# Optimization experiments

Hardware: AMD Instinct MI355X
Metric: run time of the kernel (lower is better)

The kernel has to match this reference:

```python
import jax, jax.numpy as jnp
import numpy as np

B, S, DM, H = 2, 4096, 512, 8
DEPTH = DM // H


def setup_inputs() -> dict:
    key = jax.random.key(0)
    ks = jax.random.split(key, 12)
    scale = 1.0 / np.sqrt(DM)
    return {
        "q": jax.random.normal(ks[0], (B, S, DM), jnp.float32),
        "k": jax.random.normal(ks[1], (B, S, DM), jnp.float32),
        "v": jax.random.normal(ks[2], (B, S, DM), jnp.float32),
        # padding-style mask: 1.0 = masked position, 0.0 = attend
        "mask": jax.random.bernoulli(ks[3], 0.1, (B, 1, 1, S)).astype(jnp.float32),
        "Wq": jax.random.normal(ks[4], (DM, DM), jnp.float32) * scale,
        "bq": jnp.zeros((DM,), jnp.float32),
        "Wk": jax.random.normal(ks[5], (DM, DM), jnp.float32) * scale,
        "bk": jnp.zeros((DM,), jnp.float32),
        "Wv": jax.random.normal(ks[6], (DM, DM), jnp.float32) * scale,
        "bv": jnp.zeros((DM,), jnp.float32),
        "Wo": jax.random.normal(ks[7], (DM, DM), jnp.float32) * scale,
        "bo": jnp.zeros((DM,), jnp.float32),
    }


def _split_heads(x):
    # [B, S, DM] -> [B, H, S, DEPTH]
    b, s, _ = x.shape
    return x.reshape(b, s, H, DEPTH).transpose(0, 2, 1, 3)


def reference(q, k, v, mask, Wq, bq, Wk, bk, Wv, bv, Wo, bo):
    qh = _split_heads(q @ Wq + bq)   # [B,H,S,D]
    kh = _split_heads(k @ Wk + bk)
    vh = _split_heads(v @ Wv + bv)
    logits = jnp.einsum("bhqd,bhkd->bhqk", qh, kh) / jnp.sqrt(
        jnp.asarray(DEPTH, qh.dtype))
    logits = logits + mask * (-1e9)
    attn = jax.nn.softmax(logits, axis=-1)          # [B,H,Sq,Sk]
    out = jnp.einsum("bhqk,bhkd->bhqd", attn, vh)   # [B,H,S,D]
    out = out.transpose(0, 2, 1, 3).reshape(q.shape[0], -1, DM)
    return out @ Wo + bo
```

## Files before the change

kernel.cpp:

```cpp
#include <hip/hip_runtime.h>
#include <math.h>

#define BDIM 2
#define SDIM 4096
#define DMODEL 512
#define NHEAD 8
#define DHEAD 64
#define MROWS (BDIM * SDIM)

typedef __attribute__((ext_vector_type(8))) short short8;
typedef __attribute__((ext_vector_type(4))) float f32x4;

#define MFMA16(a, b, c) __builtin_amdgcn_mfma_f32_16x16x32_bf16((a), (b), (c), 0, 0, 0)
#define EXP2F(x) __builtin_amdgcn_exp2f(x)

#define SCALE2 0.18033688011112042f
#define MASKMUL -1.442695040e9f
#define M0C 16.0f

#define GLOAD_LDS16(g, l)                                                     \
  __builtin_amdgcn_global_load_lds(                                           \
      (const __attribute__((address_space(1))) void*)(g),                     \
      (__attribute__((address_space(3))) void*)(l), 16, 0, 0)

__device__ inline void bf16_split(float x, short& h, short& l) {
  unsigned u = __float_as_uint(x);
  h = (short)(u >> 16);
  float hf = __uint_as_float(u & 0xffff0000u);
  l = (short)(__float_as_uint(x - hf) >> 16);
}

__global__ __launch_bounds__(256) void wsplit_kernel(
    const float* __restrict__ W0, const float* __restrict__ W1,
    const float* __restrict__ W2, const float* __restrict__ W3,
    short* __restrict__ T0h, short* __restrict__ T0l, short* __restrict__ T1h,
    short* __restrict__ T1l, short* __restrict__ T2h, short* __restrict__ T2l,
    short* __restrict__ T3h, short* __restrict__ T3l) {
  __shared__ short Th[64 * 72], Tl[64 * 72];
  const int tid = threadIdx.x;
  const int k0 = blockIdx.x * 64;
  const int n0 = blockIdx.y * 64;
  const int z = blockIdx.z;
  const float* W = (z == 0) ? W0 : (z == 1) ? W1 : (z == 2) ? W2 : W3;
  short* Oh = (z == 0) ? T0h : (z == 1) ? T1h : (z == 2) ? T2h : T3h;
  short* Ol = (z == 0) ? T0l : (z == 1) ? T1l : (z == 2) ? T2l : T3l;

  {
    const int r = tid >> 2;
    const int c16 = (tid & 3) * 16;
    short8 h0, h1, l0, l1;
#pragma unroll
    for (int g = 0; g < 2; g++) {
      const f32x4 a = *(const f32x4*)(W + (size_t)(k0 + r) * DMODEL + n0 + c16 + g * 8);
      const f32x4 b = *(const f32x4*)(W + (size_t)(k0 + r) * DMODEL + n0 + c16 + g * 8 + 4);
      short8& hh = g ? h1 : h0;
      short8& ll = g ? l1 : l0;
#pragma unroll
      for (int j = 0; j < 4; j++) {
        short x, y;
        bf16_split(a[j], x, y);
        hh[j] = x;
        ll[j] = y;
        bf16_split(b[j], x, y);
        hh[4 + j] = x;
        ll[4 + j] = y;
      }
    }
    *(short8*)&Th[r * 72 + c16] = h0;
    *(short8*)&Th[r * 72 + c16 + 8] = h1;
    *(short8*)&Tl[r * 72 + c16] = l0;
    *(short8*)&Tl[r * 72 + c16 + 8] = l1;
  }
  __syncthreads();
  {
    const int n = tid >> 2;
    const int kc = (tid & 3) * 16;
    short8 h0, h1, l0, l1;
#pragma unroll
    for (int i = 0; i < 8; i++) {
      h0[i] = Th[(kc + i) * 72 + n];
      h1[i] = Th[(kc + 8 + i) * 72 + n];
      l0[i] = Tl[(kc + i) * 72 + n];
      l1[i] = Tl[(kc + 8 + i) * 72 + n];
    }
    short* dh = Oh + (size_t)(n0 + n) * DMODEL + k0 + kc;
    short* dl = Ol + (size_t)(n0 + n) * DMODEL + k0 + kc;
    *(short8*)dh = h0;
    *(short8*)(dh + 8) = h1;
    *(short8*)dl = l0;
    *(short8*)(dl + 8) = l1;
  }
}

__global__ __launch_bounds__(256) void xsplit_kernel(const float* __restrict__ X,
                                                     short* __restrict__ Xh,
                                                     short* __restrict__ Xl) {
  const size_t i = ((size_t)blockIdx.x * 256 + threadIdx.x) * 8;
  const f32x4 a = *(const f32x4*)(X + i);
  const f32x4 b = *(const f32x4*)(X + i + 4);
  short8 h, l;
#pragma unroll
  for (int j = 0; j < 4; j++) {
    short x, y;
    bf16_split(a[j], x, y);
    h[j] = x;
    l[j] = y;
    bf16_split(b[j], x, y);
    h[4 + j] = x;
    l[4 + j] = y;
  }
  *(short8*)(Xh + i) = h;
  *(short8*)(Xl + i) = l;
}

template <int MODE>
__global__ __launch_bounds__(512, 2) void proj2_kernel(
    const short* __restrict__ Xh, const short* __restrict__ Xl,
    const short* __restrict__ Wth, const short* __restrict__ Wtl,
    const float* __restrict__ bias, float* __restrict__ out,
    short* __restrict__ oh, short* __restrict__ ol) {
  __shared__ short L[2 * 20480];
  const int tid = threadIdx.x;
  const int lane = tid & 63;
  const int w = tid >> 6;
  const int lane15 = lane & 15;
  const int quad = lane >> 4;
  const int m0 = blockIdx.x * 64;
  const int n0 = blockIdx.y * 256;
  const int wm = (w >> 2) * 32;
  const int wn = (w & 3) * 64;

  const short* gp[5];
  int ldso[5];
#pragma unroll
  for (int i = 0; i < 5; i++) {
    const int idx = w * 5 + i;
    const int g = idx * 64 + lane;
    if (g < 512) {
      const short* src = (g < 256) ? Xh : Xl;
      const int a = g & 255;
      gp[i] = src + (size_t)(m0 + (a >> 2)) * DMODEL + (a & 3) * 8;
    } else {
      const int gg = g - 512;
      const short* src = (gg < 1024) ? Wth : Wtl;
      const int a = gg & 1023;
      gp[i] = src + (size_t)(n0 + (a >> 2)) * DMODEL + (a & 3) * 8;
    }
    ldso[i] = idx * 512;
  }

  f32x4 c[2][4];
#pragma unroll
  for (int mt = 0; mt < 2; mt++)
#pragma unroll
    for (int nt = 0; nt < 4; nt++) c[mt][nt] = (f32x4){0.f, 0.f, 0.f, 0.f};

  constexpr int NT = DMODEL / 32;

#pragma unroll
  for (int i = 0; i < 5; i++) GLOAD_LDS16(gp[i], &L[ldso[i]]);

  for (int t = 0; t < NT; t++) {
    __syncthreads();
    if (t + 1 < NT) {
      short* dst = &L[((t + 1) & 1) * 20480];
#pragma unroll
      for (int i = 0; i < 5; i++)
        GLOAD_LDS16(gp[i] + (t + 1) * 32, dst + ldso[i]);
    }
    const short* buf = &L[(t & 1) * 20480];
    short8 ah[2], al[2], bh[4], bl[4];
#pragma unroll
    for (int mt = 0; mt < 2; mt++) {
      const int r = wm + mt * 16 + lane15;
      ah[mt] = *(const short8*)&buf[r * 32 + quad * 8];
      al[mt] = *(const short8*)&buf[2048 + r * 32 + quad * 8];
    }
#pragma unroll
    for (int nt = 0; nt < 4; nt++) {
      const int r = wn + nt * 16 + lane15;
      bh[nt] = *(const short8*)&buf[4096 + r * 32 + quad * 8];
      bl[nt] = *(const short8*)&buf[12288 + r * 32 + quad * 8];
    }
    __builtin_amdgcn_s_setprio(1);
#pragma unroll
    for (int mt = 0; mt < 2; mt++)
#pragma unroll
      for (int nt = 0; nt < 4; nt++) {
        c[mt][nt] = MFMA16(ah[mt], bh[nt], c[mt][nt]);
        c[mt][nt] = MFMA16(ah[mt], bl[nt], c[mt][nt]);
        c[mt][nt] = MFMA16(al[mt], bh[nt], c[mt][nt]);
      }
    __builtin_amdgcn_s_setprio(0);
  }

#pragma unroll
  for (int nt = 0; nt < 4; nt++) {
    const int n = n0 + wn + nt * 16 + lane15;
    const float bb = bias[n];
#pragma unroll
    for (int mt = 0; mt < 2; mt++)
#pragma unroll
      for (int r = 0; r < 4; r++) {
        const int m = m0 + wm + mt * 16 + quad * 4 + r;
        const float val = c[mt][nt][r] + bb;
        if (MODE == 1) {
          const int bidx = m >> 12;
          const int s = m & 4095;
          const int hh = n >> 6;
          const int d = n & 63;
          const size_t off =
              ((size_t)(bidx * NHEAD + hh) * SDIM + s) * DHEAD + d;
          short x, y;
          bf16_split(val, x, y);
          oh[off] = x;
          ol[off] = y;
        } else {
          out[(size_t)m * DMODEL + n] = val;
        }
      }
  }
}

__global__ __launch_bounds__(256) void vtrans_kernel(
    const short* __restrict__ vh, const short* __restrict__ vl,
    short* __restrict__ vth, short* __restrict__ vtl) {
  __shared__ short Th[64 * 72], Tl[64 * 72];
  const int tid = threadIdx.x;
  const int s0 = blockIdx.x * 64;
  const int h = blockIdx.y;
  const int b = blockIdx.z;
  const size_t base = (size_t)(b * NHEAD + h) * SDIM * DHEAD;

  {
    const int s = tid >> 2;
    const int c = tid & 3;
    const short* srcH = vh + base + (size_t)(s0 + s) * DHEAD + c * 16;
    const short* srcL = vl + base + (size_t)(s0 + s) * DHEAD + c * 16;
    *(short8*)&Th[s * 72 + c * 16] = *(const short8*)srcH;
    *(short8*)&Th[s * 72 + c * 16 + 8] = *(const short8*)(srcH + 8);
    *(short8*)&Tl[s * 72 + c * 16] = *(const short8*)srcL;
    *(short8*)&Tl[s * 72 + c * 16 + 8] = *(const short8*)(srcL + 8);
  }
  __syncthreads();
  {
    const int d = tid & 63;
    const int cw = tid >> 6;
    short8 a0, a1, b0, b1;
#pragma unroll
    for (int i = 0; i < 8; i++) {
      a0[i] = Th[(cw * 16 + i) * 72 + d];
      a1[i] = Th[(cw * 16 + 8 + i) * 72 + d];
      b0[i] = Tl[(cw * 16 + i) * 72 + d];
      b1[i] = Tl[(cw * 16 + 8 + i) * 72 + d];
    }
    short* dstH = vth + base + (size_t)d * SDIM + s0 + cw * 16;
    short* dstL = vtl + base + (size_t)d * SDIM + s0 + cw * 16;
    *(short8*)dstH = a0;
    *(short8*)(dstH + 8) = a1;
    *(short8*)dstL = b0;
    *(short8*)(dstL + 8) = b1;
  }
}

#define KP 72
#define VP 72
#define PP 68

__global__ __launch_bounds__(256, 2) void flash_attn_kernel(
    const short* __restrict__ qhh, const short* __restrict__ qhl,
    const short* __restrict__ khh, const short* __restrict__ khl,
    const short* __restrict__ vth, const short* __restrict__ vtl,
    const float* __restrict__ mask, short* __restrict__ ctxh,
    short* __restrict__ ctxl) {
  __shared__ short Ksh[64 * KP], Ksl[64 * KP];
  __shared__ short Vsh[64 * VP], Vsl[64 * VP];
  __shared__ float Ps[128 * PP];

  const int tid = threadIdx.x;
  const int lane = tid & 63;
  const int w = tid >> 6;
  const int lane15 = lane & 15;
  const int quad = lane >> 4;
  const int q0 = blockIdx.x * 128;
  const int h = blockIdx.y;
  const int b = blockIdx.z;

  const size_t base = (size_t)(b * NHEAD + h) * SDIM * DHEAD;
  const short* Qh = qhh + base;
  const short* Ql = qhl + base;
  const short* Kh = khh + base;
  const short* Kl = khl + base;
  const short* Vh = vth + base;
  const short* Vl = vtl + base;
  const float* mb = mask + (size_t)b * SDIM;

  short8 qfh[2][2], qfl[2][2];
#pragma unroll
  for (int mt = 0; mt < 2; mt++) {
    const size_t row = q0 + w * 32 + mt * 16 + lane15;
#pragma unroll
    for (int ks = 0; ks < 2; ks++) {
      qfh[mt][ks] = *(const short8*)(Qh + row * DHEAD + ks * 32 + quad * 8);
      qfl[mt][ks] = *(const short8*)(Ql + row * DHEAD + ks * 32 + quad * 8);
    }
  }

  f32x4 o[2][4];
#pragma unroll
  for (int mt = 0; mt < 2; mt++)
#pragma unroll
    for (int dt = 0; dt < 4; dt++) o[mt][dt] = (f32x4){0.f, 0.f, 0.f, 0.f};
  float lr[2][4];
#pragma unroll
  for (int mt = 0; mt < 2; mt++)
#pragma unroll
    for (int r = 0; r < 4; r++) lr[mt][r] = 0.f;

  short8 onesb;
#pragma unroll
  for (int j = 0; j < 8; j++) onesb[j] = (short)0x3F80;

  const int sr = tid >> 2;
  const int sc = (tid & 3) * 16;

  short8 rg[8];
  rg[0] = *(const short8*)(Kh + (size_t)sr * DHEAD + sc);
  rg[1] = *(const short8*)(Kh + (size_t)sr * DHEAD + sc + 8);
  rg[2] = *(const short8*)(Kl + (size_t)sr * DHEAD + sc);
  rg[3] = *(const short8*)(Kl + (size_t)sr * DHEAD + sc + 8);
  rg[4] = *(const short8*)(Vh + (size_t)sr * SDIM + sc);
  rg[5] = *(const short8*)(Vh + (size_t)sr * SDIM + sc + 8);
  rg[6] = *(const short8*)(Vl + (size_t)sr * SDIM + sc);
  rg[7] = *(const short8*)(Vl + (size_t)sr * SDIM + sc + 8);

  for (int kt = 0; kt < SDIM / 64; kt++) {
    const int k0 = kt * 64;
    __builtin_amdgcn_s_barrier();
    __builtin_amdgcn_sched_barrier(0);
    *(short8*)&Ksh[sr * KP + sc] = rg[0];
    *(short8*)&Ksh[sr * KP + sc + 8] = rg[1];
    *(short8*)&Ksl[sr * KP + sc] = rg[2];
    *(short8*)&Ksl[sr * KP + sc + 8] = rg[3];
    *(short8*)&Vsh[sr * VP + sc] = rg[4];
    *(short8*)&Vsh[sr * VP + sc + 8] = rg[5];
    *(short8*)&Vsl[sr * VP + sc] = rg[6];
    *(short8*)&Vsl[sr * VP + sc + 8] = rg[7];
    if (kt + 1 < SDIM / 64) {
      const int k1 = k0 + 64;
      rg[0] = *(const short8*)(Kh + (size_t)(k1 + sr) * DHEAD + sc);
      rg[1] = *(const short8*)(Kh + (size_t)(k1 + sr) * DHEAD + sc + 8);
      rg[2] = *(const short8*)(Kl + (size_t)(k1 + sr) * DHEAD + sc);
      rg[3] = *(const short8*)(Kl + (size_t)(k1 + sr) * DHEAD + sc + 8);
      rg[4] = *(const short8*)(Vh + (size_t)sr * SDIM + k1 + sc);
      rg[5] = *(const short8*)(Vh + (size_t)sr * SDIM + k1 + sc + 8);
      rg[6] = *(const short8*)(Vl + (size_t)sr * SDIM + k1 + sc);
      rg[7] = *(const short8*)(Vl + (size_t)sr * SDIM + k1 + sc + 8);
    }
    float mv[4];
#pragma unroll
    for (int nt = 0; nt < 4; nt++)
      mv[nt] = fmaf(mb[k0 + nt * 16 + lane15], MASKMUL, -M0C);
    asm volatile("s_waitcnt lgkmcnt(0)" ::: "memory");
    __builtin_amdgcn_s_barrier();
    __builtin_amdgcn_sched_barrier(0);

    __builtin_amdgcn_s_setprio(1);
#pragma unroll
    for (int mt = 0; mt < 2; mt++)
#pragma unroll
      for (int nt = 0; nt < 4; nt++) {
        f32x4 acc = (f32x4){0.f, 0.f, 0.f, 0.f};
#pragma unroll
        for (int ks = 0; ks < 2; ks++) {
          const int koff = (nt * 16 + lane15) * KP + ks * 32 + quad * 8;
          const short8 kbh = *(const short8*)&Ksh[koff];
          const short8 kbl = *(const short8*)&Ksl[koff];
          acc = MFMA16(qfh[mt][ks], kbh, acc);
          acc = MFMA16(qfh[mt][ks], kbl, acc);
          acc = MFMA16(qfl[mt][ks], kbh, acc);
        }
#pragma unroll
        for (int r = 0; r < 4; r++) {
          const float p = EXP2F(fmaf(acc[r], SCALE2, mv[nt]));
          Ps[(w * 32 + mt * 16 + quad * 4 + r) * PP + nt * 16 + lane15] = p;
        }
      }
    __builtin_amdgcn_s_setprio(0);

    short8 pah[2][2], pal[2][2];
#pragma unroll
    for (int mt = 0; mt < 2; mt++)
#pragma unroll
      for (int kf = 0; kf < 2; kf++) {
        const float* pr =
            &Ps[(w * 32 + mt * 16 + lane15) * PP + kf * 32 + quad * 8];
        const f32x4 p0 = *(const f32x4*)pr;
        const f32x4 p1 = *(const f32x4*)(pr + 4);
        short8 ph, pl;
#pragma unroll
        for (int j = 0; j < 4; j++) {
          short hh, ll;
          bf16_split(p0[j], hh, ll);
          ph[j] = hh;
          pl[j] = ll;
        }
#pragma unroll
        for (int j = 0; j < 4; j++) {
          short hh, ll;
          bf16_split(p1[j], hh, ll);
          ph[4 + j] = hh;
          pl[4 + j] = ll;
        }
        pah[mt][kf] = ph;
        pal[mt][kf] = pl;
      }

    __builtin_amdgcn_s_setprio(1);
#pragma unroll
    for (int mt = 0; mt < 2; mt++) {
      f32x4 racc = (f32x4){0.f, 0.f, 0.f, 0.f};
#pragma unroll
      for (int kf = 0; kf < 2; kf++) {
        racc = MFMA16(pah[mt][kf], onesb, racc);
        racc = MFMA16(pal[mt][kf], onesb, racc);
      }
#pragma unroll
      for (int r = 0; r < 4; r++) lr[mt][r] += racc[r];
    }

#pragma unroll
    for (int dt = 0; dt < 4; dt++)
#pragma unroll
      for (int kf = 0; kf < 2; kf++) {
        const int voff = (dt * 16 + lane15) * VP + kf * 32 + quad * 8;
        const short8 vbh = *(const short8*)&Vsh[voff];
        const short8 vbl = *(const short8*)&Vsl[voff];
#pragma unroll
        for (int mt = 0; mt < 2; mt++) {
          o[mt][dt] = MFMA16(pah[mt][kf], vbh, o[mt][dt]);
          o[mt][dt] = MFMA16(pah[mt][kf], vbl, o[mt][dt]);
          o[mt][dt] = MFMA16(pal[mt][kf], vbh, o[mt][dt]);
        }
      }
    __builtin_amdgcn_s_setprio(0);
  }

  float inv[2][4];
#pragma unroll
  for (int mt = 0; mt < 2; mt++)
#pragma unroll
    for (int r = 0; r < 4; r++) inv[mt][r] = 1.f / lr[mt][r];
#pragma unroll
  for (int mt = 0; mt < 2; mt++)
#pragma unroll
    for (int dt = 0; dt < 4; dt++)
#pragma unroll
      for (int r = 0; r < 4; r++) {
        const int q = q0 + w * 32 + mt * 16 + quad * 4 + r;
        const int col = h * DHEAD + dt * 16 + lane15;
        const float val = o[mt][dt][r] * inv[mt][r];
        short x, y;
        bf16_split(val, x, y);
        const size_t off = ((size_t)b * SDIM + q) * DMODEL + col;
        ctxh[off] = x;
        ctxl[off] = y;
      }
}

extern "C" void kernel_launch(void* const* d_in, const int* in_sizes, int n_in,
                              void* d_out, int out_size, void* d_ws,
                              size_t ws_size, hipStream_t stream) {
  const float* q = (const float*)d_in[0];
  const float* k = (const float*)d_in[1];
  const float* v = (const float*)d_in[2];
  const float* mask = (const float*)d_in[3];
  const float* Wq = (const float*)d_in[4];
  const float* bq = (const float*)d_in[5];
  const float* Wk = (const float*)d_in[6];
  const float* bk = (const float*)d_in[7];
  const float* Wv = (const float*)d_in[8];
  const float* bv = (const float*)d_in[9];
  const float* Wo = (const float*)d_in[10];
  const float* bo = (const float*)d_in[11];
  float* out = (float*)d_out;

  char* W = (char*)d_ws;
  const size_t SZB = (size_t)MROWS * DMODEL * sizeof(short);
  short* q_h = (short*)(W + 0 * SZB);
  short* q_l = (short*)(W + 1 * SZB);
  short* k_h = (short*)(W + 2 * SZB);
  short* k_l = (short*)(W + 3 * SZB);
  short* v_h = (short*)(W + 4 * SZB);
  short* v_l = (short*)(W + 5 * SZB);
  short* vt_h = (short*)(W + 6 * SZB);
  short* vt_l = (short*)(W + 7 * SZB);
  short* cx_h = (short*)(W + 8 * SZB);
  short* cx_l = (short*)(W + 9 * SZB);
  const size_t WSZ = (size_t)DMODEL * DMODEL * sizeof(short);
  char* WT = W + 10 * SZB;
  short* wtq_h = (short*)(WT + 0 * WSZ);
  short* wtq_l = (short*)(WT + 1 * WSZ);
  short* wtk_h = (short*)(WT + 2 * WSZ);
  short* wtk_l = (short*)(WT + 3 * WSZ);
  short* wtv_h = (short*)(WT + 4 * WSZ);
  short* wtv_l = (short*)(WT + 5 * WSZ);
  short* wto_h = (short*)(WT + 6 * WSZ);
  short* wto_l = (short*)(WT + 7 * WSZ);

  wsplit_kernel<<<dim3(DMODEL / 64, DMODEL / 64, 4), 256, 0, stream>>>(
      Wq, Wk, Wv, Wo, wtq_h, wtq_l, wtk_h, wtk_l, wtv_h, wtv_l, wto_h, wto_l);

  const dim3 gx(MROWS * DMODEL / (256 * 8));
  const dim3 gp2(MROWS / 64, DMODEL / 256);

  xsplit_kernel<<<gx, 256, 0, stream>>>(q, cx_h, cx_l);
  proj2_kernel<1><<<gp2, 512, 0, stream>>>(cx_h, cx_l, wtq_h, wtq_l, bq,
                                           nullptr, q_h, q_l);
  xsplit_kernel<<<gx, 256, 0, stream>>>(k, cx_h, cx_l);
  proj2_kernel<1><<<gp2, 512, 0, stream>>>(cx_h, cx_l, wtk_h, wtk_l, bk,
                                           nullptr, k_h, k_l);
  xsplit_kernel<<<gx, 256, 0, stream>>>(v, cx_h, cx_l);
  proj2_kernel<1><<<gp2, 512, 0, stream>>>(cx_h, cx_l, wtv_h, wtv_l, bv,
                                           nullptr, v_h, v_l);

  vtrans_kernel<<<dim3(SDIM / 64, NHEAD, BDIM), 256, 0, stream>>>(v_h, v_l,
                                                                  vt_h, vt_l);

  flash_attn_kernel<<<dim3(SDIM / 128, NHEAD, BDIM), 256, 0, stream>>>(
      q_h, q_l, k_h, k_l, vt_h, vt_l, mask, cx_h, cx_l);

  proj2_kernel<0><<<gp2, 512, 0, stream>>>(cx_h, cx_l, wto_h, wto_l, bo, out,
                                           nullptr, nullptr);
}
```

Measured before the change: 415.3 us.

## Fuse fp32 split into projection GEMM and load K/V directly in flash attention

```diff
diff --git a/kernel.cpp b/kernel.cpp
--- a/kernel.cpp
+++ b/kernel.cpp
@@ -92,33 +92,11 @@
   }
 }
 
-__global__ __launch_bounds__(256) void xsplit_kernel(const float* __restrict__ X,
-                                                     short* __restrict__ Xh,
-                                                     short* __restrict__ Xl) {
-  const size_t i = ((size_t)blockIdx.x * 256 + threadIdx.x) * 8;
-  const f32x4 a = *(const f32x4*)(X + i);
-  const f32x4 b = *(const f32x4*)(X + i + 4);
-  short8 h, l;
-#pragma unroll
-  for (int j = 0; j < 4; j++) {
-    short x, y;
-    bf16_split(a[j], x, y);
-    h[j] = x;
-    l[j] = y;
-    bf16_split(b[j], x, y);
-    h[4 + j] = x;
-    l[4 + j] = y;
-  }
-  *(short8*)(Xh + i) = h;
-  *(short8*)(Xl + i) = l;
-}
-
 template <int MODE>
-__global__ __launch_bounds__(512, 2) void proj2_kernel(
-    const short* __restrict__ Xh, const short* __restrict__ Xl,
-    const short* __restrict__ Wth, const short* __restrict__ Wtl,
-    const float* __restrict__ bias, float* __restrict__ out,
-    short* __restrict__ oh, short* __restrict__ ol) {
+__global__ __launch_bounds__(512, 2) void proj3_kernel(
+    const float* __restrict__ X, const short* __restrict__ Wth,
+    const short* __restrict__ Wtl, const float* __restrict__ bias,
+    float* __restrict__ out, short* __restrict__ oh, short* __restrict__ ol) {
   __shared__ short L[2 * 20480];
   const int tid = threadIdx.x;
   const int lane = tid & 63;
@@ -130,21 +108,21 @@
   const int wm = (w >> 2) * 32;
   const int wn = (w & 3) * 64;
 
-  const short* gp[5];
-  int ldso[5];
+  const char* gp[5];
+  int stepb[5], ldso[5];
 #pragma unroll
   for (int i = 0; i < 5; i++) {
     const int idx = w * 5 + i;
-    const int g = idx * 64 + lane;
-    if (g < 512) {
-      const short* src = (g < 256) ? Xh : Xl;
-      const int a = g & 255;
-      gp[i] = src + (size_t)(m0 + (a >> 2)) * DMODEL + (a & 3) * 8;
+    if (idx < 8) {
+      const int g = idx * 64 + lane;
+      gp[i] = (const char*)(X + (size_t)(m0 + (g >> 3)) * DMODEL + (g & 7) * 4);
+      stepb[i] = 128;
     } else {
-      const int gg = g - 512;
+      const int gg = idx * 64 + lane - 512;
       const short* src = (gg < 1024) ? Wth : Wtl;
       const int a = gg & 1023;
-      gp[i] = src + (size_t)(n0 + (a >> 2)) * DMODEL + (a & 3) * 8;
+      gp[i] = (const char*)(src + (size_t)(n0 + (a >> 2)) * DMODEL + (a & 3) * 8);
+      stepb[i] = 64;
     }
     ldso[i] = idx * 512;
   }
@@ -166,15 +144,26 @@
       short* dst = &L[((t + 1) & 1) * 20480];
 #pragma unroll
       for (int i = 0; i < 5; i++)
-        GLOAD_LDS16(gp[i] + (t + 1) * 32, dst + ldso[i]);
+        GLOAD_LDS16(gp[i] + (t + 1) * stepb[i], dst + ldso[i]);
     }
     const short* buf = &L[(t & 1) * 20480];
+    const float* Af = (const float*)buf;
     short8 ah[2], al[2], bh[4], bl[4];
 #pragma unroll
     for (int mt = 0; mt < 2; mt++) {
       const int r = wm + mt * 16 + lane15;
-      ah[mt] = *(const short8*)&buf[r * 32 + quad * 8];
-      al[mt] = *(const short8*)&buf[2048 + r * 32 + quad * 8];
+      const f32x4 a0 = *(const f32x4*)&Af[r * 32 + quad * 8];
+      const f32x4 a1 = *(const f32x4*)&Af[r * 32 + quad * 8 + 4];
+#pragma unroll
+      for (int j = 0; j < 4; j++) {
+        short x, y;
+        bf16_split(a0[j], x, y);
+        ah[mt][j] = x;
+        al[mt][j] = y;
+        bf16_split(a1[j], x, y);
+        ah[mt][4 + j] = x;
+        al[mt][4 + j] = y;
+      }
     }
 #pragma unroll
     for (int nt = 0; nt < 4; nt++) {
@@ -263,18 +252,13 @@
   }
 }
 
-#define KP 72
-#define VP 72
 #define PP 68
 
 __global__ __launch_bounds__(256, 2) void flash_attn_kernel(
     const short* __restrict__ qhh, const short* __restrict__ qhl,
     const short* __restrict__ khh, const short* __restrict__ khl,
     const short* __restrict__ vth, const short* __restrict__ vtl,
-    const float* __restrict__ mask, short* __restrict__ ctxh,
-    short* __restrict__ ctxl) {
-  __shared__ short Ksh[64 * KP], Ksl[64 * KP];
-  __shared__ short Vsh[64 * VP], Vsl[64 * VP];
+    const float* __restrict__ mask, float* __restrict__ ctx) {
   __shared__ float Ps[128 * PP];
 
   const int tid = threadIdx.x;
@@ -282,9 +266,12 @@
   const int w = tid >> 6;
   const int lane15 = lane & 15;
   const int quad = lane >> 4;
-  const int q0 = blockIdx.x * 128;
-  const int h = blockIdx.y;
-  const int b = blockIdx.z;
+
+  const int bid = blockIdx.x + (SDIM / 128) * (blockIdx.y + NHEAD * blockIdx.z);
+  const int sw = (bid & 7) * 64 + (bid >> 3);
+  const int q0 = (sw & 31) * 128;
+  const int h = (sw >> 5) & 7;
+  const int b = sw >> 8;
 
   const size_t base = (size_t)(b * NHEAD + h) * SDIM * DHEAD;
   const short* Qh = qhh + base;
@@ -321,49 +308,23 @@
 #pragma unroll
   for (int j = 0; j < 8; j++) onesb[j] = (short)0x3F80;
 
-  const int sr = tid >> 2;
-  const int sc = (tid & 3) * 16;
-
-  short8 rg[8];
-  rg[0] = *(const short8*)(Kh + (size_t)sr * DHEAD + sc);
-  rg[1] = *(const short8*)(Kh + (size_t)sr * DHEAD + sc + 8);
-  rg[2] = *(const short8*)(Kl + (size_t)sr * DHEAD + sc);
-  rg[3] = *(const short8*)(Kl + (size_t)sr * DHEAD + sc + 8);
-  rg[4] = *(const short8*)(Vh + (size_t)sr * SDIM + sc);
-  rg[5] = *(const short8*)(Vh + (size_t)sr * SDIM + sc + 8);
-  rg[6] = *(const short8*)(Vl + (size_t)sr * SDIM + sc);
-  rg[7] = *(const short8*)(Vl + (size_t)sr * SDIM + sc + 8);
-
   for (int kt = 0; kt < SDIM / 64; kt++) {
     const int k0 = kt * 64;
-    __builtin_amdgcn_s_barrier();
-    __builtin_amdgcn_sched_barrier(0);
-    *(short8*)&Ksh[sr * KP + sc] = rg[0];
-    *(short8*)&Ksh[sr * KP + sc + 8] = rg[1];
-    *(short8*)&Ksl[sr * KP + sc] = rg[2];
-    *(short8*)&Ksl[sr * KP + sc + 8] = rg[3];
-    *(short8*)&Vsh[sr * VP + sc] = rg[4];
-    *(short8*)&Vsh[sr * VP + sc + 8] = rg[5];
-    *(short8*)&Vsl[sr * VP + sc] = rg[6];
-    *(short8*)&Vsl[sr * VP + sc + 8] = rg[7];
-    if (kt + 1 < SDIM / 64) {
-      const int k1 = k0 + 64;
-      rg[0] = *(const short8*)(Kh + (size_t)(k1 + sr) * DHEAD + sc);
-      rg[1] = *(const short8*)(Kh + (size_t)(k1 + sr) * DHEAD + sc + 8);
-      rg[2] = *(const short8*)(Kl + (size_t)(k1 + sr) * DHEAD + sc);
-      rg[3] = *(const short8*)(Kl + (size_t)(k1 + sr) * DHEAD + sc + 8);
-      rg[4] = *(const short8*)(Vh + (size_t)sr * SDIM + k1 + sc);
-      rg[5] = *(const short8*)(Vh + (size_t)sr * SDIM + k1 + sc + 8);
-      rg[6] = *(const short8*)(Vl + (size_t)sr * SDIM + k1 + sc);
-      rg[7] = *(const short8*)(Vl + (size_t)sr * SDIM + k1 + sc + 8);
-    }
+
+    short8 kh8[4][2], kl8[4][2];
+#pragma unroll
+    for (int nt = 0; nt < 4; nt++)
+#pragma unroll
+      for (int ks = 0; ks < 2; ks++) {
+        const size_t ko =
+            (size_t)(k0 + nt * 16 + lane15) * DHEAD + ks * 32 + quad * 8;
+        kh8[nt][ks] = *(const short8*)(Kh + ko);
+        kl8[nt][ks] = *(const short8*)(Kl + ko);
+      }
     float mv[4];
 #pragma unroll
     for (int nt = 0; nt < 4; nt++)
       mv[nt] = fmaf(mb[k0 + nt * 16 + lane15], MASKMUL, -M0C);
-    asm volatile("s_waitcnt lgkmcnt(0)" ::: "memory");
-    __builtin_amdgcn_s_barrier();
-    __builtin_amdgcn_sched_barrier(0);
 
     __builtin_amdgcn_s_setprio(1);
 #pragma unroll
@@ -373,12 +334,9 @@
         f32x4 acc = (f32x4){0.f, 0.f, 0.f, 0.f};
 #pragma unroll
         for (int ks = 0; ks < 2; ks++) {
-          const int koff = (nt * 16 + lane15) * KP + ks * 32 + quad * 8;
-          const short8 kbh = *(const short8*)&Ksh[koff];
-          const short8 kbl = *(const short8*)&Ksl[koff];
-          acc = MFMA16(qfh[mt][ks], kbh, acc);
-          acc = MFMA16(qfh[mt][ks], kbl, acc);
-          acc = MFMA16(qfl[mt][ks], kbh, acc);
+          acc = MFMA16(qfh[mt][ks], kh8[nt][ks], acc);
+          acc = MFMA16(qfh[mt][ks], kl8[nt][ks], acc);
+          acc = MFMA16(qfl[mt][ks], kh8[nt][ks], acc);
         }
 #pragma unroll
         for (int r = 0; r < 4; r++) {
@@ -387,6 +345,17 @@
         }
       }
     __builtin_amdgcn_s_setprio(0);
+
+    short8 vh8[4][2], vl8[4][2];
+#pragma unroll
+    for (int dt = 0; dt < 4; dt++)
+#pragma unroll
+      for (int kf = 0; kf < 2; kf++) {
+        const size_t vo =
+            (size_t)(dt * 16 + lane15) * SDIM + k0 + kf * 32 + quad * 8;
+        vh8[dt][kf] = *(const short8*)(Vh + vo);
+        vl8[dt][kf] = *(const short8*)(Vl + vo);
+      }
 
     short8 pah[2][2], pal[2][2];
 #pragma unroll
@@ -433,14 +402,11 @@
     for (int dt = 0; dt < 4; dt++)
 #pragma unroll
       for (int kf = 0; kf < 2; kf++) {
-        const int voff = (dt * 16 + lane15) * VP + kf * 32 + quad * 8;
-        const short8 vbh = *(const short8*)&Vsh[voff];
-        const short8 vbl = *(const short8*)&Vsl[voff];
 #pragma unroll
         for (int mt = 0; mt < 2; mt++) {
-          o[mt][dt] = MFMA16(pah[mt][kf], vbh, o[mt][dt]);
-          o[mt][dt] = MFMA16(pah[mt][kf], vbl, o[mt][dt]);
-          o[mt][dt] = MFMA16(pal[mt][kf], vbh, o[mt][dt]);
+          o[mt][dt] = MFMA16(pah[mt][kf], vh8[dt][kf], o[mt][dt]);
+          o[mt][dt] = MFMA16(pah[mt][kf], vl8[dt][kf], o[mt][dt]);
+          o[mt][dt] = MFMA16(pal[mt][kf], vh8[dt][kf], o[mt][dt]);
         }
       }
     __builtin_amdgcn_s_setprio(0);
@@ -459,12 +425,7 @@
       for (int r = 0; r < 4; r++) {
         const int q = q0 + w * 32 + mt * 16 + quad * 4 + r;
         const int col = h * DHEAD + dt * 16 + lane15;
-        const float val = o[mt][dt][r] * inv[mt][r];
-        short x, y;
-        bf16_split(val, x, y);
-        const size_t off = ((size_t)b * SDIM + q) * DMODEL + col;
-        ctxh[off] = x;
-        ctxl[off] = y;
+        ctx[((size_t)b * SDIM + q) * DMODEL + col] = o[mt][dt][r] * inv[mt][r];
       }
 }
 
@@ -495,10 +456,9 @@
   short* v_l = (short*)(W + 5 * SZB);
   short* vt_h = (short*)(W + 6 * SZB);
   short* vt_l = (short*)(W + 7 * SZB);
-  short* cx_h = (short*)(W + 8 * SZB);
-  short* cx_l = (short*)(W + 9 * SZB);
+  float* ctx = (float*)(W + 4 * SZB);
   const size_t WSZ = (size_t)DMODEL * DMODEL * sizeof(short);
-  char* WT = W + 10 * SZB;
+  char* WT = W + 8 * SZB;
   short* wtq_h = (short*)(WT + 0 * WSZ);
   short* wtq_l = (short*)(WT + 1 * WSZ);
   short* wtk_h = (short*)(WT + 2 * WSZ);
@@ -511,25 +471,21 @@
   wsplit_kernel<<<dim3(DMODEL / 64, DMODEL / 64, 4), 256, 0, stream>>>(
       Wq, Wk, Wv, Wo, wtq_h, wtq_l, wtk_h, wtk_l, wtv_h, wtv_l, wto_h, wto_l);
 
-  const dim3 gx(MROWS * DMODEL / (256 * 8));
   const dim3 gp2(MROWS / 64, DMODEL / 256);
 
-  xsplit_kernel<<<gx, 256, 0, stream>>>(q, cx_h, cx_l);
-  proj2_kernel<1><<<gp2, 512, 0, stream>>>(cx_h, cx_l, wtq_h, wtq_l, bq,
-                                           nullptr, q_h, q_l);
-  xsplit_kernel<<<gx, 256, 0, stream>>>(k, cx_h, cx_l);
-  proj2_kernel<1><<<gp2, 512, 0, stream>>>(cx_h, cx_l, wtk_h, wtk_l, bk,
-                                           nullptr, k_h, k_l);
-  xsplit_kernel<<<gx, 256, 0, stream>>>(v, cx_h, cx_l);
-  proj2_kernel<1><<<gp2, 512, 0, stream>>>(cx_h, cx_l, wtv_h, wtv_l, bv,
-                                           nullptr, v_h, v_l);
+  proj3_kernel<1><<<gp2, 512, 0, stream>>>(q, wtq_h, wtq_l, bq, nullptr, q_h,
+                                           q_l);
+  proj3_kernel<1><<<gp2, 512, 0, stream>>>(k, wtk_h, wtk_l, bk, nullptr, k_h,
+                                           k_l);
+  proj3_kernel<1><<<gp2, 512, 0, stream>>>(v, wtv_h, wtv_l, bv, nullptr, v_h,
+                                           v_l);
 
   vtrans_kernel<<<dim3(SDIM / 64, NHEAD, BDIM), 256, 0, stream>>>(v_h, v_l,
                                                                   vt_h, vt_l);
 
   flash_attn_kernel<<<dim3(SDIM / 128, NHEAD, BDIM), 256, 0, stream>>>(
-      q_h, q_l, k_h, k_l, vt_h, vt_l, mask, cx_h, cx_l);
-
-  proj2_kernel<0><<<gp2, 512, 0, stream>>>(cx_h, cx_l, wto_h, wto_l, bo, out,
-                                           nullptr, nullptr);
-}
+      q_h, q_l, k_h, k_l, vt_h, vt_l, mask, ctx);
+
+  proj3_kernel<0><<<gp2, 512, 0, stream>>>(ctx, wto_h, wto_l, bo, out, nullptr,
+                                           nullptr);
+}
```

New measurement: 655.3 us. 57.8% more time.
